# Kernel tuning notes

Hardware: AMD Instinct MI355X
Metric: run time of the kernel (lower is better)

The kernel has to match this reference:

```python
import jax, jax.numpy as jnp
import numpy as np
from jax import lax

# --- Clifford algebra Cl(3,0): sig_g = [1,1,1], n_blades = 8 ---
SIG = np.array([1.0, 1.0, 1.0], dtype=np.float32)
N_GEN = len(SIG)
N_BLADES = 1 << N_GEN

def _build_cayley(g):
    # Structure constants C[a,b,c]: e_a * e_b = C[a,b,a^b] * e_{a^b}
    n = len(g); nb = 1 << n
    C = np.zeros((nb, nb, nb), dtype=np.float32)
    for a in range(nb):
        for b in range(nb):
            s = 1.0
            x = a >> 1
            while x:
                if bin(x & b).count('1') % 2:
                    s = -s
                x >>= 1
            common = a & b
            for k in range(n):
                if (common >> k) & 1:
                    s *= g[k]
            C[a, b, a ^ b] = s
    return C

CAYLEY = _build_cayley(SIG)
# blade signs: scalar coefficient of e_i * e_i (metric square of each blade)
BLADE_SIGNS = np.array([CAYLEY[i, i, 0] for i in range(N_BLADES)], dtype=np.float32)

DT = 0.1      # EPEngine dt
N_FREE = 5    # EPEngine n_free

def _energy(h, input_mv, W_rec, C, signs):
    # h: [B,L,H,I]
    rho = jnp.clip(h, 0.0, 1.0)
    E_self = 0.5 * jnp.sum(h * h, axis=(1, 2, 3))                       # [B]
    E_in = jnp.einsum('blhi,blhi,i->b', rho, input_mv, signs)           # [B]
    # causal recurrent term: geometric product of h_{l-1} with W_rec
    rec = jnp.einsum('blhi,ghj,ijk->blgk', rho[:, :-1], W_rec, C)       # [B,L-1,H,I]
    E_rec = jnp.einsum('blhk,blhk,k->b', rho[:, 1:], rec, signs)        # [B]
    return E_self - E_in - E_rec

def _free_phase(h0, input_mv, W_rec, C, signs):
    gfn = jax.grad(lambda h: jnp.sum(_energy(h, input_mv, W_rec, C, signs)))
    def step(h, _):
        return h - DT * gfn(h), None
    h, _ = lax.scan(step, h0, None, length=N_FREE)
    return h

def setup_inputs() -> dict:
    key = jax.random.key(0)
    ks = jax.random.split(key, 5)
    B, L, V, E, H = 4, 256, 32000, 256, 256
    x = jax.random.randint(ks[0], (B, L), 0, V)
    emb_table = jax.random.normal(ks[1], (V, E), jnp.float32)
    W_in = jax.random.normal(ks[2], (H, E, N_BLADES), jnp.float32) * 0.1
    W_rec = jax.random.normal(ks[3], (H, H, N_BLADES), jnp.float32) * 0.05
    W_out = jax.random.normal(ks[4], (V, H, N_BLADES), jnp.float32) * 0.1
    return {"x": x, "emb_table": emb_table, "W_in": W_in, "W_rec": W_rec, "W_out": W_out}

def reference(x, emb_table, W_in, W_rec, W_out):
    C = jnp.asarray(CAYLEY)
    signs = jnp.asarray(BLADE_SIGNS)
    emb = emb_table[x]                                  # [B,L,E]
    input_mv = jnp.einsum('bld,hdi->blhi', emb, W_in)   # [B,L,H,I]
    B, L = x.shape
    H = W_in.shape[0]
    h0 = jnp.zeros((B, L, H, N_BLADES), jnp.float32)
    h_free = _free_phase(h0, input_mv, W_rec, C, signs) # [B,L,H,I]
    # scalar part of geometric product of h_free with W_out (only blade 0 kept)
    logits = jnp.einsum('blhi,vhj,ij->blv', h_free, W_out, C[:, :, 0])
    return logits
```

## Files before the change

### kernel.cpp

```cpp
#include <hip/hip_runtime.h>
#include <cstddef>
#include <cstdint>

#define VOCAB  32000
#define EMB    256
#define NB     8
#define KDIM   2048
#define NROWS  1024
#define NCOL   4096
#define LLEN   256

typedef __attribute__((ext_vector_type(8))) short short8;
typedef __attribute__((ext_vector_type(4))) float f32x4;
typedef __attribute__((ext_vector_type(16))) float f32x16;
typedef __attribute__((ext_vector_type(4))) int i32x4;
typedef __attribute__((ext_vector_type(16))) int i32x16;

__device__ __forceinline__ float cl3_sign(int a, int b) {
  int x = a >> 1, p = 0;
  while (x) { p ^= __popc(x & b) & 1; x >>= 1; }
  return p ? -1.f : 1.f;
}

__device__ __forceinline__ float clipf(float v) { return fminf(fmaxf(v, 0.f), 1.f); }

__device__ __forceinline__ unsigned short f2bf(float f) {
  unsigned u = __float_as_uint(f);
  u += 0x7FFF + ((u >> 16) & 1);
  return (unsigned short)(u >> 16);
}
__device__ __forceinline__ float bf2f(unsigned short h) {
  return __uint_as_float(((unsigned)h) << 16);
}

__device__ __forceinline__ void gload16(const void* g, void* l) {
  __builtin_amdgcn_global_load_lds((const __attribute__((address_space(1))) uint32_t*)g,
                                   (__attribute__((address_space(3))) uint32_t*)l, 16, 0, 0);
}

__device__ __forceinline__ float dig_inv(float mx) {
  return exp2f((float)(5 - ilogbf(fmaxf(mx, 1e-20f))));
}

__device__ __forceinline__ size_t bfoff(int rt, int k, int r) {
  return ((size_t)(rt * 128 + (k >> 4)) << 11) + (size_t)(((k >> 3) & 1) << 10) + ((r & 127) << 3) + (k & 7);
}

__global__ void k_build_mrt_split(const float* __restrict__ Wrec,
                                  unsigned short* __restrict__ Mhi,
                                  unsigned short* __restrict__ Mlo) {
  int idx = blockIdx.x * blockDim.x + threadIdx.x;
  int k = idx & (KDIM - 1);
  int n = idx >> 11;
  int h = k >> 3, i = k & 7;
  float v;
  if (n < KDIM) {
    int g = n >> 3, kb = n & 7;
    int j = i ^ kb;
    v = Wrec[(size_t)g * KDIM + h * NB + j] * cl3_sign(i, j);
  } else {
    int c = n - KDIM;
    int p = c >> 3, q = c & 7;
    int j = q ^ i;
    v = cl3_sign(i, i) * cl3_sign(q, j) * Wrec[(size_t)h * KDIM + p * NB + j];
  }
  unsigned short hi = f2bf(v);
  unsigned short lo = f2bf(v - bf2f(hi));
  size_t off = bfoff(n >> 7, k, n);
  Mhi[off] = hi; Mlo[off] = lo;
}

__global__ __launch_bounds__(256) void k_dig_wout(const float* __restrict__ W,
                                                  float* __restrict__ sB,
                                                  char* __restrict__ Wd1,
                                                  char* __restrict__ Wd2) {
  __shared__ float ld[4 * 2052];
  __shared__ float rmax[4];
  const int t = threadIdx.x;
  const int bid = blockIdx.x;
  const float* src = W + (size_t)bid * 8192;
#pragma unroll
  for (int i = 0; i < 8; ++i) {
    int f = i * 256 + t;
    int row = f >> 9, c4 = f & 511;
    float4 v = ((const float4*)src)[f];
    *(float4*)&ld[row * 2052 + c4 * 4] = v;
  }
  __syncthreads();
  const int w = t >> 6, l = t & 63;
  float m = 0.f;
#pragma unroll
  for (int j = 0; j < 8; ++j) {
    float4 v = *(const float4*)&ld[w * 2052 + (j * 64 + l) * 4];
    m = fmaxf(m, fmaxf(fmaxf(fabsf(v.x), fabsf(v.y)), fmaxf(fabsf(v.z), fabsf(v.w))));
  }
#pragma unroll
  for (int s = 1; s < 64; s <<= 1) m = fmaxf(m, __shfl_xor(m, s));
  m = fmaxf(m, 1e-20f);
  if (l == 0) { rmax[w] = m; sB[bid * 4 + w] = exp2f((float)(ilogbf(m) + 2)); }
  __syncthreads();
  const int rloc = t & 3;
  const int rowg = bid * 4 + rloc;
  const int rowtile = rowg >> 7, rowin = rowg & 127;
  const float inv = dig_inv(rmax[rloc]);
#pragma unroll
  for (int it = 0; it < 2; ++it) {
    int c16 = (t >> 2) + it * 64;
    char d1[16], d2[16];
#pragma unroll
    for (int j = 0; j < 16; ++j) {
      float tv = ld[rloc * 2052 + c16 * 16 + j] * inv;
      float f1 = rintf(tv);
      d1[j] = (char)(int)f1;
      d2[j] = (char)(int)rintf((tv - f1) * 128.f);
    }
    size_t addr = ((size_t)(rowtile * 64 + (c16 >> 1)) << 12) + (size_t)((c16 & 1) << 11) + (rowin << 4);
    *(i32x4*)&Wd1[addr] = *(i32x4*)d1;
    *(i32x4*)&Wd2[addr] = *(i32x4*)d2;
  }
}

__global__ __launch_bounds__(256) void k_input_h1(const int* __restrict__ x,
                                                  const float* __restrict__ emb,
                                                  const float* __restrict__ Win,
                                                  float* __restrict__ Imv,
                                                  float* __restrict__ Hb,
                                                  unsigned short* __restrict__ Hhi,
                                                  unsigned short* __restrict__ Hlo) {
  __shared__ float se[4][EMB];
  int r0 = blockIdx.x * 4;
  int t = threadIdx.x;
  for (int rr = 0; rr < 4; ++rr) {
    int tok = x[r0 + rr];
    se[rr][t] = emb[(size_t)tok * EMB + t];
  }
  __syncthreads();
  float acc[4][8];
#pragma unroll
  for (int rr = 0; rr < 4; ++rr)
#pragma unroll
    for (int i = 0; i < 8; ++i) acc[rr][i] = 0.f;
  const float* wrow = Win + (size_t)t * KDIM;
  for (int d = 0; d < EMB; ++d) {
    float4 w0 = *(const float4*)(wrow + d * 8);
    float4 w1 = *(const float4*)(wrow + d * 8 + 4);
#pragma unroll
    for (int rr = 0; rr < 4; ++rr) {
      float e = se[rr][d];
      acc[rr][0] += e * w0.x; acc[rr][1] += e * w0.y;
      acc[rr][2] += e * w0.z; acc[rr][3] += e * w0.w;
      acc[rr][4] += e * w1.x; acc[rr][5] += e * w1.y;
      acc[rr][6] += e * w1.z; acc[rr][7] += e * w1.w;
    }
  }
  const int c = t * 8;
  for (int rr = 0; rr < 4; ++rr) {
    int r = r0 + rr;
    float* o = Imv + (size_t)r * KDIM + c;
    *(float4*)o = make_float4(acc[rr][0], acc[rr][1], acc[rr][2], acc[rr][3]);
    *(float4*)(o + 4) = make_float4(acc[rr][4], acc[rr][5], acc[rr][6], acc[rr][7]);
    float hn[8];
    short8 h8, l8;
#pragma unroll
    for (int j = 0; j < 8; ++j) {
      float f = acc[rr][j] * (((0xE8 >> j) & 1) ? -1.f : 1.f);
      hn[j] = 0.f - 0.1f * (0.f - 0.5f * f);
      float a = clipf(hn[j]);
      unsigned short hi = f2bf(a);
      h8[j] = (short)hi;
      l8[j] = (short)f2bf(a - bf2f(hi));
    }
    float* hb = Hb + (size_t)r * KDIM + c;
    *(float4*)hb = make_float4(hn[0], hn[1], hn[2], hn[3]);
    *(float4*)(hb + 4) = make_float4(hn[4], hn[5], hn[6], hn[7]);
    size_t off = bfoff(r >> 7, c, r);
    *(short8*)&Hhi[off] = h8;
    *(short8*)&Hlo[off] = l8;
  }
}

__global__ __launch_bounds__(256, 4) void k_gemm_pre(const unsigned short* __restrict__ Ahi,
                                                     const unsigned short* __restrict__ Alo,
                                                     const unsigned short* __restrict__ Bhi,
                                                     const unsigned short* __restrict__ Blo,
                                                     float* __restrict__ RF0,
                                                     float* __restrict__ RF1) {
  __shared__ __align__(16) char lds[3 * 12288];
  const int b = blockIdx.x;
  const int lin = (b & 7) * 128 + (b >> 3);
  const int tm = lin & 7;
  const int rest = lin >> 3;
  const int tn = rest & 63, half = rest >> 6;
  const int ktbase = half * 64;
  float* __restrict__ C = half ? RF1 : RF0;
  const int t = threadIdx.x;
  const int l = t & 63, w = t >> 6;
  const int wr = w >> 1, wc = w & 1;
  const int wo = w << 10;

  const char* aHg = (const char*)Ahi + (((size_t)(tm * 128 + ktbase)) << 12) + (t << 4);
  const char* aLg = (const char*)Alo + (((size_t)(tm * 128 + ktbase)) << 12) + (t << 4);
  const int jj = t & 127;
  const int bt = tn >> 1, r0b = (tn & 1) << 6;
  const char* bGg = (const char*)((t >> 7) ? Blo : Bhi)
                  + (((size_t)(bt * 128 + ktbase)) << 12)
                  + ((jj >> 6) << 11) + ((size_t)(r0b + (jj & 63)) << 4);

  f32x16 acc[2];
  acc[0] = (f32x16)0.f; acc[1] = (f32x16)0.f;

  auto STAGE = [&](int bf, int kt) {
    char* lb = &lds[bf * 12288];
    size_t kb = (size_t)kt << 12;
    gload16(aHg + kb, lb + wo);
    gload16(aLg + kb, lb + 4096 + wo);
    gload16(bGg + kb, lb + 8192 + wo);
  };

  STAGE(0, 0); STAGE(1, 1);

  const int ra = wr * 64 + (l & 31);
  const int rb = wc * 32 + (l & 31);
  const int kq = l >> 5;
  int cur = 0;
  for (int kt = 0; kt < 64; ++kt) {
    int pf = cur + 2; if (pf >= 3) pf -= 3;
    if (kt < 63) { asm volatile("s_waitcnt vmcnt(3)" ::: "memory"); }
    else         { asm volatile("s_waitcnt vmcnt(0)" ::: "memory"); }
    __builtin_amdgcn_s_barrier();
    const char* lb = &lds[cur * 12288];
    short8 ah[2], al[2], bh, bl;
#pragma unroll
    for (int mi = 0; mi < 2; ++mi) {
      int off = (kq << 11) + ((ra + mi * 32) << 4);
      ah[mi] = *(const short8*)(lb + off);
      al[mi] = *(const short8*)(lb + 4096 + off);
    }
    {
      int off = (kq << 10) + (rb << 4);
      bh = *(const short8*)(lb + 8192 + off);
      bl = *(const short8*)(lb + 10240 + off);
    }
    if (kt + 2 < 64) STAGE(pf, kt + 2);
    __builtin_amdgcn_s_setprio(1);
#pragma unroll
    for (int mi = 0; mi < 2; ++mi) {
      acc[mi] = __builtin_amdgcn_mfma_f32_32x32x16_bf16(ah[mi], bh, acc[mi], 0, 0, 0);
      acc[mi] = __builtin_amdgcn_mfma_f32_32x32x16_bf16(ah[mi], bl, acc[mi], 0, 0, 0);
      acc[mi] = __builtin_amdgcn_mfma_f32_32x32x16_bf16(al[mi], bh, acc[mi], 0, 0, 0);
    }
    __builtin_amdgcn_s_setprio(0);
    cur = (cur == 2) ? 0 : cur + 1;
  }

  const int rg0 = tm * 128 + wr * 64 + ((l >> 5) << 2);
  const int cg0 = tn * 64 + wc * 32 + (l & 31);
#pragma unroll
  for (int mi = 0; mi < 2; ++mi) {
    f32x16 v = acc[mi];
#pragma unroll
    for (int g = 0; g < 16; ++g) {
      int rr = (g & 3) + ((g >> 2) << 3);
      C[(size_t)(rg0 + mi * 32 + rr) * NCOL + cg0] = v[g];
    }
  }
}

__global__ __launch_bounds__(256, 3) void k_gemm_i8(const char* __restrict__ Ad1,
                                                    const char* __restrict__ Ad2,
                                                    const char* __restrict__ Bd1,
                                                    const char* __restrict__ Bd2,
                                                    const float* __restrict__ sA,
                                                    const float* __restrict__ sB,
                                                    float* __restrict__ C) {
  __shared__ __align__(16) char lds[3 * 12288];
  const int b = blockIdx.x;
  const int lin = (b & 7) * 500 + (b >> 3);
  const int tm = lin & 7, tn = lin >> 3;
  const int t = threadIdx.x;
  const int l = t & 63, w = t >> 6;
  const int wr = w >> 1, wc = w & 1;
  const int wo = w << 10;

  const char* a1g = Ad1 + (((size_t)tm * 64) << 12) + (t << 4);
  const char* a2g = Ad2 + (((size_t)tm * 64) << 12) + (t << 4);
  const int jj = t & 127;
  const int wt = tn >> 1, r0b = (tn & 1) << 6;
  const char* bGg = ((t >> 7) ? Bd2 : Bd1)
                  + (((size_t)wt * 64) << 12)
                  + ((jj >> 6) << 11) + ((size_t)(r0b + (jj & 63)) << 4);

  i32x16 acc1[2], acc2[2];
  acc1[0] = (i32x16)0; acc1[1] = (i32x16)0;
  acc2[0] = (i32x16)0; acc2[1] = (i32x16)0;

  auto STAGE = [&](int bf, int kt) {
    char* lb = &lds[bf * 12288];
    size_t kb = (size_t)kt << 12;
    gload16(a1g + kb, lb + wo);
    gload16(a2g + kb, lb + 4096 + wo);
    gload16(bGg + kb, lb + 8192 + wo);
  };

  STAGE(0, 0); STAGE(1, 1);

  const int ra = wr * 64 + (l & 31);
  const int rb = wc * 32 + (l & 31);
  const int kq = l >> 5;
  int cur = 0;
  for (int kt = 0; kt < 64; ++kt) {
    int pf = cur + 2; if (pf >= 3) pf -= 3;
    if (kt < 63) { asm volatile("s_waitcnt vmcnt(3)" ::: "memory"); }
    else         { asm volatile("s_waitcnt vmcnt(0)" ::: "memory"); }
    __builtin_amdgcn_s_barrier();
    const char* lb = &lds[cur * 12288];
    i32x4 a1[2], a2[2], b1, b2;
#pragma unroll
    for (int mi = 0; mi < 2; ++mi) {
      int off = (kq << 11) + ((ra + mi * 32) << 4);
      a1[mi] = *(const i32x4*)(lb + off);
      a2[mi] = *(const i32x4*)(lb + 4096 + off);
    }
    {
      int off = (kq << 10) + (rb << 4);
      b1 = *(const i32x4*)(lb + 8192 + off);
      b2 = *(const i32x4*)(lb + 10240 + off);
    }
    if (kt + 2 < 64) STAGE(pf, kt + 2);
    __builtin_amdgcn_s_setprio(1);
#pragma unroll
    for (int mi = 0; mi < 2; ++mi) {
      acc1[mi] = __builtin_amdgcn_mfma_i32_32x32x32_i8(a1[mi], b1, acc1[mi], 0, 0, 0);
      acc2[mi] = __builtin_amdgcn_mfma_i32_32x32x32_i8(a1[mi], b2, acc2[mi], 0, 0, 0);
      acc2[mi] = __builtin_amdgcn_mfma_i32_32x32x32_i8(a2[mi], b1, acc2[mi], 0, 0, 0);
    }
    __builtin_amdgcn_s_setprio(0);
    cur = (cur == 2) ? 0 : cur + 1;
  }

  const int rbase = tm * 128 + wr * 64 + ((l >> 5) << 2);
  const int cb = tn * 64 + wc * 32 + (l & 31);
  const float sBv = sB[cb] * (1.f / 16384.f);
#pragma unroll
  for (int mi = 0; mi < 2; ++mi) {
#pragma unroll
    for (int g = 0; g < 16; ++g) {
      int rr = (g & 3) + ((g >> 2) << 3);
      int row = rbase + mi * 32 + rr;
      float c1 = sA[row] * sBv;
      C[(size_t)row * VOCAB + cb] =
          fmaf((float)acc2[mi][g], c1 * (1.f / 128.f), (float)acc1[mi][g] * c1);
    }
  }
}

template <int LAST>
__global__ __launch_bounds__(256) void k_update(float* __restrict__ Hb, const float* __restrict__ Imv,
                                                const float* __restrict__ RF0, const float* __restrict__ RF1,
                                                unsigned short* __restrict__ Hhi,
                                                unsigned short* __restrict__ Hlo,
                                                float* __restrict__ sA,
                                                char* __restrict__ Ad1,
                                                char* __restrict__ Ad2,
                                                int big) {
  __shared__ float red[256];
  int tix = threadIdx.x;
  int idx = blockIdx.x * 256 + tix;
  int r = idx >> 8;
  int c = (idx & 255) << 3;
  int m = r & (LLEN - 1);
  const size_t base = (size_t)r * KDIM + c;
  float h[8], f[8];
  *(float4*)&h[0] = *(const float4*)(Hb + base);
  *(float4*)&h[4] = *(const float4*)(Hb + base + 4);
  float4 i0 = *(const float4*)(Imv + base);
  float4 i1 = *(const float4*)(Imv + base + 4);
  f[0] = i0.x; f[1] = i0.y; f[2] = i0.z; f[3] = i0.w;
  f[4] = i1.x; f[5] = i1.y; f[6] = i1.z; f[7] = i1.w;
#pragma unroll
  for (int j = 0; j < 8; ++j) f[j] *= ((0xE8 >> j) & 1) ? -1.f : 1.f;
  if (m >= 1) {
    const float* rp0 = RF0 + (size_t)(r - 1) * NCOL + c;
    const float* rp1 = RF1 + (size_t)(r - 1) * NCOL + c;
#pragma unroll
    for (int j = 0; j < 8; ++j)
      f[j] += (rp0[j] + rp1[j]) * (((0xE8 >> j) & 1) ? -1.f : 1.f);
  }
  if (m < LLEN - 1) {
    const float* rn0 = RF0 + (size_t)(r + 1) * NCOL + KDIM + c;
    const float* rn1 = RF1 + (size_t)(r + 1) * NCOL + KDIM + c;
#pragma unroll
    for (int j = 0; j < 8; ++j) f[j] += rn0[j] + rn1[j];
  }
  float hn[8], av[8];
#pragma unroll
  for (int j = 0; j < 8; ++j) {
    float hv = h[j];
    float dr = (hv > 0.f && hv < 1.f) ? 1.f : ((hv == 0.f || hv == 1.f) ? 0.5f : 0.f);
    hn[j] = hv - 0.1f * (hv - dr * f[j]);
  }
  *(float4*)(Hb + base) = make_float4(hn[0], hn[1], hn[2], hn[3]);
  *(float4*)(Hb + base + 4) = make_float4(hn[4], hn[5], hn[6], hn[7]);
  if (!LAST) {
    short8 h8, l8;
#pragma unroll
    for (int j = 0; j < 8; ++j) {
      float a = clipf(hn[j]);
      unsigned short hi = f2bf(a);
      h8[j] = (short)hi;
      l8[j] = (short)f2bf(a - bf2f(hi));
    }
    size_t off = bfoff(r >> 7, c, r);
    *(short8*)&Hhi[off] = h8;
    *(short8*)&Hlo[off] = l8;
  } else {
    if (!big) return;
#pragma unroll
    for (int j = 0; j < 8; ++j) av[j] = hn[j] * (((0xE8 >> j) & 1) ? -1.f : 1.f);
    float lm = 0.f;
#pragma unroll
    for (int j = 0; j < 8; ++j) lm = fmaxf(lm, fabsf(av[j]));
    red[tix] = lm; __syncthreads();
    for (int s = 128; s; s >>= 1) { if (tix < s) red[tix] = fmaxf(red[tix], red[tix + s]); __syncthreads(); }
    float mx = fmaxf(red[0], 1e-20f);
    float inv = dig_inv(mx);
    if (tix == 0) sA[r] = exp2f((float)(ilogbf(mx) + 2));
    char d1[8], d2[8];
#pragma unroll
    for (int j = 0; j < 8; ++j) {
      float tv = av[j] * inv;
      float f1 = rintf(tv);
      d1[j] = (char)(int)f1;
      d2[j] = (char)(int)rintf((tv - f1) * 128.f);
    }
    size_t addr = ((size_t)((r >> 7) * 64 + (c >> 5)) << 12) + (size_t)(((c >> 4) & 1) << 11)
                + ((r & 127) << 4) + (c & 15);
    *(uint64_t*)&Ad1[addr] = *(uint64_t*)d1;
    *(uint64_t*)&Ad2[addr] = *(uint64_t*)d2;
  }
}

template <int AMODE>
__global__ __launch_bounds__(256) void k_gemm_split(const float* __restrict__ A,
                                                    const float* __restrict__ B,
                                                    float* __restrict__ C, int ldc) {
  __shared__ unsigned short Ah[128 * 32], Al[128 * 32];
  __shared__ unsigned short Bh[128 * 32], Bl[128 * 32];
  const int t = threadIdx.x;
  const int row0 = blockIdx.y * 128, col0 = blockIdx.x * 128;
  const int l = t & 63, w = t >> 6;
  const int wr = w >> 1, wc = w & 1;
  const int sr = t >> 3;
  const int cc = (t & 7) << 2;
  const int chunkb = cc >> 3;
  const int halfo = (cc >> 2) & 1;
  f32x4 acc[4][4];
#pragma unroll
  for (int i = 0; i < 4; ++i)
#pragma unroll
    for (int j = 0; j < 4; ++j) acc[i][j] = (f32x4)0.f;
  const float sA0 = 1.f;
  const float sA1 = (cc & 4) ? -1.f : 1.f;
  const float sA2 = sA1;
  const float sA3 = -1.f;
  for (int k0 = 0; k0 < KDIM; k0 += 32) {
    float4 va[4], vb[4];
#pragma unroll
    for (int i = 0; i < 4; ++i) {
      va[i] = *(const float4*)(A + (size_t)(row0 + sr + i * 32) * KDIM + k0 + cc);
      vb[i] = *(const float4*)(B + (size_t)(col0 + sr + i * 32) * KDIM + k0 + cc);
    }
    __syncthreads();
#pragma unroll
    for (int i = 0; i < 4; ++i) {
      int row = sr + i * 32;
      int idx = row * 32 + ((chunkb ^ (row & 3)) << 3) + (halfo << 2);
      float4 a = va[i];
      if (AMODE == 0) {
        a.x = clipf(a.x); a.y = clipf(a.y); a.z = clipf(a.z); a.w = clipf(a.w);
      } else {
        a.x *= sA0; a.y *= sA1; a.z *= sA2; a.w *= sA3;
      }
      ushort4 h4, l4;
      h4.x = f2bf(a.x); l4.x = f2bf(a.x - bf2f(h4.x));
      h4.y = f2bf(a.y); l4.y = f2bf(a.y - bf2f(h4.y));
      h4.z = f2bf(a.z); l4.z = f2bf(a.z - bf2f(h4.z));
      h4.w = f2bf(a.w); l4.w = f2bf(a.w - bf2f(h4.w));
      *(ushort4*)&Ah[idx] = h4;
      *(ushort4*)&Al[idx] = l4;
      float4 bb = vb[i];
      h4.x = f2bf(bb.x); l4.x = f2bf(bb.x - bf2f(h4.x));
      h4.y = f2bf(bb.y); l4.y = f2bf(bb.y - bf2f(h4.y));
      h4.z = f2bf(bb.z); l4.z = f2bf(bb.z - bf2f(h4.z));
      h4.w = f2bf(bb.w); l4.w = f2bf(bb.w - bf2f(h4.w));
      *(ushort4*)&Bh[idx] = h4;
      *(ushort4*)&Bl[idx] = l4;
    }
    __syncthreads();
    short8 ah[4], al[4], bh[4], bl[4];
#pragma unroll
    for (int mi = 0; mi < 4; ++mi) {
      int ar = wr * 64 + mi * 16 + (l & 15);
      int kc = (l >> 4) ^ (ar & 3);
      ah[mi] = *(short8*)&Ah[ar * 32 + kc * 8];
      al[mi] = *(short8*)&Al[ar * 32 + kc * 8];
      int br = wc * 64 + mi * 16 + (l & 15);
      int kb = (l >> 4) ^ (br & 3);
      bh[mi] = *(short8*)&Bh[br * 32 + kb * 8];
      bl[mi] = *(short8*)&Bl[br * 32 + kb * 8];
    }
#pragma unroll
    for (int mi = 0; mi < 4; ++mi)
#pragma unroll
      for (int ni = 0; ni < 4; ++ni) {
        acc[mi][ni] = __builtin_amdgcn_mfma_f32_16x16x32_bf16(ah[mi], bh[ni], acc[mi][ni], 0, 0, 0);
        acc[mi][ni] = __builtin_amdgcn_mfma_f32_16x16x32_bf16(ah[mi], bl[ni], acc[mi][ni], 0, 0, 0);
        acc[mi][ni] = __builtin_amdgcn_mfma_f32_16x16x32_bf16(al[mi], bh[ni], acc[mi][ni], 0, 0, 0);
      }
  }
#pragma unroll
  for (int mi = 0; mi < 4; ++mi)
#pragma unroll
    for (int ni = 0; ni < 4; ++ni) {
      int rg = row0 + wr * 64 + mi * 16 + (l >> 4) * 4;
      int cg = col0 + wc * 64 + ni * 16 + (l & 15);
#pragma unroll
      for (int j = 0; j < 4; ++j)
        C[(size_t)(rg + j) * ldc + cg] = acc[mi][ni][j];
    }
}

extern "C" void kernel_launch(void* const* d_in, const int* in_sizes, int n_in,
                              void* d_out, int out_size, void* d_ws, size_t ws_size,
                              hipStream_t stream) {
  const int*   x    = (const int*)d_in[0];
  const float* emb  = (const float*)d_in[1];
  const float* Win  = (const float*)d_in[2];
  const float* Wrec = (const float*)d_in[3];
  const float* Wout = (const float*)d_in[4];
  float* logits = (float*)d_out;

  char* base = (char*)d_ws;
  const size_t MB = 1ull << 20;
  float* Hbuf = (float*)(base + 0);
  float* Imv  = (float*)(base + 8 * MB);
  float* RF0  = (float*)(base + 16 * MB);
  float* RF1  = (float*)(base + 32 * MB);
  unsigned short* Hhi = (unsigned short*)(base + 48 * MB);
  unsigned short* Hlo = (unsigned short*)(base + 52 * MB);
  unsigned short* Mhi = (unsigned short*)(base + 56 * MB);
  unsigned short* Mlo = (unsigned short*)(base + 72 * MB);
  float* sA  = (float*)(base + 88 * MB);
  float* sB  = (float*)(base + 88 * MB + 4096);
  char* Wd1  = base + 88 * MB + 160 * 1024;
  char* Wd2  = Wd1 + (size_t)VOCAB * KDIM;
  char* Ad1  = (char*)Mhi;
  char* Ad2  = (char*)Mlo;

  const size_t need = (size_t)(Wd2 - base) + (size_t)VOCAB * KDIM;
  const bool big = ws_size >= need;

  k_build_mrt_split<<<32768, 256, 0, stream>>>(Wrec, Mhi, Mlo);
  k_input_h1<<<256, 256, 0, stream>>>(x, emb, Win, Imv, Hbuf, Hhi, Hlo);
  if (big) {
    k_dig_wout<<<8000, 256, 0, stream>>>(Wout, sB, Wd1, Wd2);
  }

  for (int it = 1; it < 5; ++it) {
    k_gemm_pre<<<1024, 256, 0, stream>>>(Hhi, Hlo, Mhi, Mlo, RF0, RF1);
    if (it < 4) k_update<0><<<1024, 256, 0, stream>>>(Hbuf, Imv, RF0, RF1, Hhi, Hlo, sA, Ad1, Ad2, big);
    else        k_update<1><<<1024, 256, 0, stream>>>(Hbuf, Imv, RF0, RF1, Hhi, Hlo, sA, Ad1, Ad2, big);
  }

  if (big) {
    k_gemm_i8<<<4000, 256, 0, stream>>>(Ad1, Ad2, Wd1, Wd2, sA, sB, logits);
  } else {
    k_gemm_split<1><<<dim3(VOCAB / 128, NROWS / 128), 256, 0, stream>>>(Hbuf, Wout, logits, VOCAB);
  }
}
```

Baseline: 694.9 us.

## Enlarge GEMM block tiles to 128x128 with 512-thread blocks

```diff
diff --git a/kernel.cpp b/kernel.cpp
--- a/kernel.cpp
+++ b/kernel.cpp
@@ -179,177 +179,169 @@
   }
 }
 
-__global__ __launch_bounds__(256, 4) void k_gemm_pre(const unsigned short* __restrict__ Ahi,
+__global__ __launch_bounds__(512, 4) void k_gemm_pre(const unsigned short* __restrict__ Ahi,
                                                      const unsigned short* __restrict__ Alo,
                                                      const unsigned short* __restrict__ Bhi,
                                                      const unsigned short* __restrict__ Blo,
                                                      float* __restrict__ RF0,
                                                      float* __restrict__ RF1) {
-  __shared__ __align__(16) char lds[3 * 12288];
+  __shared__ __align__(16) char lds[3 * 16384];
   const int b = blockIdx.x;
-  const int lin = (b & 7) * 128 + (b >> 3);
+  const int lin = (b & 7) * 64 + (b >> 3);
   const int tm = lin & 7;
   const int rest = lin >> 3;
-  const int tn = rest & 63, half = rest >> 6;
+  const int tn = rest & 31, half = rest >> 5;
   const int ktbase = half * 64;
   float* __restrict__ C = half ? RF1 : RF0;
   const int t = threadIdx.x;
   const int l = t & 63, w = t >> 6;
-  const int wr = w >> 1, wc = w & 1;
-  const int wo = w << 10;
-
-  const char* aHg = (const char*)Ahi + (((size_t)(tm * 128 + ktbase)) << 12) + (t << 4);
-  const char* aLg = (const char*)Alo + (((size_t)(tm * 128 + ktbase)) << 12) + (t << 4);
-  const int jj = t & 127;
-  const int bt = tn >> 1, r0b = (tn & 1) << 6;
-  const char* bGg = (const char*)((t >> 7) ? Blo : Bhi)
-                  + (((size_t)(bt * 128 + ktbase)) << 12)
-                  + ((jj >> 6) << 11) + ((size_t)(r0b + (jj & 63)) << 4);
+  const int vr = w >> 1, vc = w & 1;
+  const int wo = (w & 3) << 10;
+  const int dsto = w << 10;
+
+  const char* aG = (const char*)((w >> 2) ? Alo : Ahi)
+                 + (((size_t)(tm * 128 + ktbase)) << 12) + wo + (l << 4);
+  const char* bG = (const char*)((w >> 2) ? Blo : Bhi)
+                 + (((size_t)(tn * 128 + ktbase)) << 12) + wo + (l << 4);
 
   f32x16 acc[2];
   acc[0] = (f32x16)0.f; acc[1] = (f32x16)0.f;
 
   auto STAGE = [&](int bf, int kt) {
-    char* lb = &lds[bf * 12288];
+    char* lb = &lds[bf * 16384];
     size_t kb = (size_t)kt << 12;
-    gload16(aHg + kb, lb + wo);
-    gload16(aLg + kb, lb + 4096 + wo);
-    gload16(bGg + kb, lb + 8192 + wo);
+    gload16(aG + kb, lb + dsto);
+    gload16(bG + kb, lb + 8192 + dsto);
   };
 
   STAGE(0, 0); STAGE(1, 1);
 
-  const int ra = wr * 64 + (l & 31);
-  const int rb = wc * 32 + (l & 31);
+  const int row = vr * 32 + (l & 31);
+  const int colb = vc * 64 + (l & 31);
   const int kq = l >> 5;
   int cur = 0;
   for (int kt = 0; kt < 64; ++kt) {
     int pf = cur + 2; if (pf >= 3) pf -= 3;
-    if (kt < 63) { asm volatile("s_waitcnt vmcnt(3)" ::: "memory"); }
+    if (kt < 63) { asm volatile("s_waitcnt vmcnt(2)" ::: "memory"); }
     else         { asm volatile("s_waitcnt vmcnt(0)" ::: "memory"); }
     __builtin_amdgcn_s_barrier();
-    const char* lb = &lds[cur * 12288];
-    short8 ah[2], al[2], bh, bl;
-#pragma unroll
-    for (int mi = 0; mi < 2; ++mi) {
-      int off = (kq << 11) + ((ra + mi * 32) << 4);
-      ah[mi] = *(const short8*)(lb + off);
-      al[mi] = *(const short8*)(lb + 4096 + off);
-    }
+    const char* lb = &lds[cur * 16384];
+    short8 ah, al, bh[2], bl[2];
     {
-      int off = (kq << 10) + (rb << 4);
-      bh = *(const short8*)(lb + 8192 + off);
-      bl = *(const short8*)(lb + 10240 + off);
+      int off = (kq << 11) + (row << 4);
+      ah = *(const short8*)(lb + off);
+      al = *(const short8*)(lb + 4096 + off);
+    }
+#pragma unroll
+    for (int nj = 0; nj < 2; ++nj) {
+      int off = (kq << 11) + ((colb + nj * 32) << 4);
+      bh[nj] = *(const short8*)(lb + 8192 + off);
+      bl[nj] = *(const short8*)(lb + 12288 + off);
     }
     if (kt + 2 < 64) STAGE(pf, kt + 2);
     __builtin_amdgcn_s_setprio(1);
 #pragma unroll
-    for (int mi = 0; mi < 2; ++mi) {
-      acc[mi] = __builtin_amdgcn_mfma_f32_32x32x16_bf16(ah[mi], bh, acc[mi], 0, 0, 0);
-      acc[mi] = __builtin_amdgcn_mfma_f32_32x32x16_bf16(ah[mi], bl, acc[mi], 0, 0, 0);
-      acc[mi] = __builtin_amdgcn_mfma_f32_32x32x16_bf16(al[mi], bh, acc[mi], 0, 0, 0);
+    for (int nj = 0; nj < 2; ++nj) {
+      acc[nj] = __builtin_amdgcn_mfma_f32_32x32x16_bf16(ah, bh[nj], acc[nj], 0, 0, 0);
+      acc[nj] = __builtin_amdgcn_mfma_f32_32x32x16_bf16(ah, bl[nj], acc[nj], 0, 0, 0);
+      acc[nj] = __builtin_amdgcn_mfma_f32_32x32x16_bf16(al, bh[nj], acc[nj], 0, 0, 0);
     }
     __builtin_amdgcn_s_setprio(0);
     cur = (cur == 2) ? 0 : cur + 1;
   }
 
-  const int rg0 = tm * 128 + wr * 64 + ((l >> 5) << 2);
-  const int cg0 = tn * 64 + wc * 32 + (l & 31);
-#pragma unroll
-  for (int mi = 0; mi < 2; ++mi) {
-    f32x16 v = acc[mi];
+  const int rg0 = tm * 128 + vr * 32 + ((l >> 5) << 2);
+  const int cg0 = tn * 128 + vc * 64 + (l & 31);
+#pragma unroll
+  for (int nj = 0; nj < 2; ++nj) {
+    f32x16 v = acc[nj];
 #pragma unroll
     for (int g = 0; g < 16; ++g) {
       int rr = (g & 3) + ((g >> 2) << 3);
-      C[(size_t)(rg0 + mi * 32 + rr) * NCOL + cg0] = v[g];
-    }
-  }
-}
-
-__global__ __launch_bounds__(256, 3) void k_gemm_i8(const char* __restrict__ Ad1,
+      C[(size_t)(rg0 + rr) * NCOL + cg0 + nj * 32] = v[g];
+    }
+  }
+}
+
+__global__ __launch_bounds__(512, 4) void k_gemm_i8(const char* __restrict__ Ad1,
                                                     const char* __restrict__ Ad2,
                                                     const char* __restrict__ Bd1,
                                                     const char* __restrict__ Bd2,
                                                     const float* __restrict__ sA,
                                                     const float* __restrict__ sB,
                                                     float* __restrict__ C) {
-  __shared__ __align__(16) char lds[3 * 12288];
+  __shared__ __align__(16) char lds[3 * 16384];
   const int b = blockIdx.x;
-  const int lin = (b & 7) * 500 + (b >> 3);
+  const int lin = (b & 7) * 250 + (b >> 3);
   const int tm = lin & 7, tn = lin >> 3;
   const int t = threadIdx.x;
   const int l = t & 63, w = t >> 6;
-  const int wr = w >> 1, wc = w & 1;
-  const int wo = w << 10;
-
-  const char* a1g = Ad1 + (((size_t)tm * 64) << 12) + (t << 4);
-  const char* a2g = Ad2 + (((size_t)tm * 64) << 12) + (t << 4);
-  const int jj = t & 127;
-  const int wt = tn >> 1, r0b = (tn & 1) << 6;
-  const char* bGg = ((t >> 7) ? Bd2 : Bd1)
-                  + (((size_t)wt * 64) << 12)
-                  + ((jj >> 6) << 11) + ((size_t)(r0b + (jj & 63)) << 4);
+  const int vr = w >> 1, vc = w & 1;
+  const int wo = (w & 3) << 10;
+  const int dsto = w << 10;
+
+  const char* aG = ((w >> 2) ? Ad2 : Ad1) + (((size_t)tm * 64) << 12) + wo + (l << 4);
+  const char* bG = ((w >> 2) ? Bd2 : Bd1) + (((size_t)tn * 64) << 12) + wo + (l << 4);
 
   i32x16 acc1[2], acc2[2];
   acc1[0] = (i32x16)0; acc1[1] = (i32x16)0;
   acc2[0] = (i32x16)0; acc2[1] = (i32x16)0;
 
   auto STAGE = [&](int bf, int kt) {
-    char* lb = &lds[bf * 12288];
+    char* lb = &lds[bf * 16384];
     size_t kb = (size_t)kt << 12;
-    gload16(a1g + kb, lb + wo);
-    gload16(a2g + kb, lb + 4096 + wo);
-    gload16(bGg + kb, lb + 8192 + wo);
+    gload16(aG + kb, lb + dsto);
+    gload16(bG + kb, lb + 8192 + dsto);
   };
 
   STAGE(0, 0); STAGE(1, 1);
 
-  const int ra = wr * 64 + (l & 31);
-  const int rb = wc * 32 + (l & 31);
+  const int row = vr * 32 + (l & 31);
+  const int colb = vc * 64 + (l & 31);
   const int kq = l >> 5;
   int cur = 0;
   for (int kt = 0; kt < 64; ++kt) {
     int pf = cur + 2; if (pf >= 3) pf -= 3;
-    if (kt < 63) { asm volatile("s_waitcnt vmcnt(3)" ::: "memory"); }
+    if (kt < 63) { asm volatile("s_waitcnt vmcnt(2)" ::: "memory"); }
     else         { asm volatile("s_waitcnt vmcnt(0)" ::: "memory"); }
     __builtin_amdgcn_s_barrier();
-    const char* lb = &lds[cur * 12288];
-    i32x4 a1[2], a2[2], b1, b2;
-#pragma unroll
-    for (int mi = 0; mi < 2; ++mi) {
-      int off = (kq << 11) + ((ra + mi * 32) << 4);
-      a1[mi] = *(const i32x4*)(lb + off);
-      a2[mi] = *(const i32x4*)(lb + 4096 + off);
-    }
+    const char* lb = &lds[cur * 16384];
+    i32x4 a1, a2, b1[2], b2[2];
     {
-      int off = (kq << 10) + (rb << 4);
-      b1 = *(const i32x4*)(lb + 8192 + off);
-      b2 = *(const i32x4*)(lb + 10240 + off);
+      int off = (kq << 11) + (row << 4);
+      a1 = *(const i32x4*)(lb + off);
+      a2 = *(const i32x4*)(lb + 4096 + off);
+    }
+#pragma unroll
+    for (int nj = 0; nj < 2; ++nj) {
+      int off = (kq << 11) + ((colb + nj * 32) << 4);
+      b1[nj] = *(const i32x4*)(lb + 8192 + off);
+      b2[nj] = *(const i32x4*)(lb + 12288 + off);
     }
     if (kt + 2 < 64) STAGE(pf, kt + 2);
     __builtin_amdgcn_s_setprio(1);
 #pragma unroll
-    for (int mi = 0; mi < 2; ++mi) {
-      acc1[mi] = __builtin_amdgcn_mfma_i32_32x32x32_i8(a1[mi], b1, acc1[mi], 0, 0, 0);
-      acc2[mi] = __builtin_amdgcn_mfma_i32_32x32x32_i8(a1[mi], b2, acc2[mi], 0, 0, 0);
-      acc2[mi] = __builtin_amdgcn_mfma_i32_32x32x32_i8(a2[mi], b1, acc2[mi], 0, 0, 0);
+    for (int nj = 0; nj < 2; ++nj) {
+      acc1[nj] = __builtin_amdgcn_mfma_i32_32x32x32_i8(a1, b1[nj], acc1[nj], 0, 0, 0);
+      acc2[nj] = __builtin_amdgcn_mfma_i32_32x32x32_i8(a1, b2[nj], acc2[nj], 0, 0, 0);
+      acc2[nj] = __builtin_amdgcn_mfma_i32_32x32x32_i8(a2, b1[nj], acc2[nj], 0, 0, 0);
     }
     __builtin_amdgcn_s_setprio(0);
     cur = (cur == 2) ? 0 : cur + 1;
   }
 
-  const int rbase = tm * 128 + wr * 64 + ((l >> 5) << 2);
-  const int cb = tn * 64 + wc * 32 + (l & 31);
-  const float sBv = sB[cb] * (1.f / 16384.f);
-#pragma unroll
-  for (int mi = 0; mi < 2; ++mi) {
+  const int rbase = tm * 128 + vr * 32 + ((l >> 5) << 2);
+  const int cb = tn * 128 + vc * 64 + (l & 31);
+#pragma unroll
+  for (int nj = 0; nj < 2; ++nj) {
+    float sBv = sB[cb + nj * 32] * (1.f / 16384.f);
 #pragma unroll
     for (int g = 0; g < 16; ++g) {
       int rr = (g & 3) + ((g >> 2) << 3);
-      int row = rbase + mi * 32 + rr;
-      float c1 = sA[row] * sBv;
-      C[(size_t)row * VOCAB + cb] =
-          fmaf((float)acc2[mi][g], c1 * (1.f / 128.f), (float)acc1[mi][g] * c1);
+      int row2 = rbase + rr;
+      float c1 = sA[row2] * sBv;
+      C[(size_t)row2 * VOCAB + cb + nj * 32] =
+          fmaf((float)acc2[nj][g], c1 * (1.f / 128.f), (float)acc1[nj][g] * c1);
     }
   }
 }
@@ -567,13 +559,13 @@
   }
 
   for (int it = 1; it < 5; ++it) {
-    k_gemm_pre<<<1024, 256, 0, stream>>>(Hhi, Hlo, Mhi, Mlo, RF0, RF1);
+    k_gemm_pre<<<512, 512, 0, stream>>>(Hhi, Hlo, Mhi, Mlo, RF0, RF1);
     if (it < 4) k_update<0><<<1024, 256, 0, stream>>>(Hbuf, Imv, RF0, RF1, Hhi, Hlo, sA, Ad1, Ad2, big);
     else        k_update<1><<<1024, 256, 0, stream>>>(Hbuf, Imv, RF0, RF1, Hhi, Hlo, sA, Ad1, Ad2, big);
   }
 
   if (big) {
-    k_gemm_i8<<<4000, 256, 0, stream>>>(Ad1, Ad2, Wd1, Wd2, sA, sB, logits);
+    k_gemm_i8<<<2000, 512, 0, stream>>>(Ad1, Ad2, Wd1, Wd2, sA, sB, logits);
   } else {
     k_gemm_split<1><<<dim3(VOCAB / 128, NROWS / 128), 256, 0, stream>>>(Hbuf, Wout, logits, VOCAB);
   }
```

After: 659.8 us. 1.05x faster.
